# Optimization experiments

Measured on AMD Instinct MI355X. Metric: run time of the kernel, lower is better.

Reference implementation:

```python
import jax, jax.numpy as jnp
import numpy as np

N = 100000
E = 1600000
IN_DIM = 128
H = 64
OUT_DIM = 64
EPS = 1e-5


def batch_norm(x, gamma, beta):
    # BatchNorm1d with batch statistics (training-mode normalization, biased var)
    mu = jnp.mean(x, axis=0)
    var = jnp.var(x, axis=0)
    return (x - mu) * jax.lax.rsqrt(var + EPS) * gamma + beta


def gcn_conv(x, src, dst, W, b, n_nodes):
    # PyG GCNConv: add self-loops, symmetric deg^-1/2 normalization, X W, scatter-add, bias
    loop = jnp.arange(n_nodes, dtype=src.dtype)
    s = jnp.concatenate([src, loop])
    d = jnp.concatenate([dst, loop])
    w = jnp.ones(s.shape[0], dtype=x.dtype)
    deg = jax.ops.segment_sum(w, d, num_segments=n_nodes)
    dinv = jnp.where(deg > 0, jax.lax.rsqrt(deg), 0.0)
    norm = dinv[s] * w * dinv[d]                      # [E+N]
    h = x @ W                                         # [N, out]
    msg = h[s] * norm[:, None]                        # [E+N, out]
    out = jax.ops.segment_sum(msg, d, num_segments=n_nodes)
    return out + b


def setup_inputs() -> dict:
    key = jax.random.key(0)
    ks = jax.random.split(key, 12)
    x = jax.random.normal(ks[0], (N, IN_DIM), dtype=jnp.float32)
    edge_index = jax.random.randint(ks[1], (2, E), 0, N, dtype=jnp.int64)
    s = 0.05
    return {
        "x": x,
        "edge_index": edge_index,
        "bn_in_g": jnp.ones((IN_DIM,), jnp.float32),
        "bn_in_b": jnp.zeros((IN_DIM,), jnp.float32),
        "Wp": jax.random.normal(ks[2], (IN_DIM, H), jnp.float32) * s,
        "bp": jnp.zeros((H,), jnp.float32),
        "W1": jax.random.normal(ks[3], (H, H), jnp.float32) * s,
        "b1": jnp.zeros((H,), jnp.float32),
        "bn1_g": jnp.ones((H,), jnp.float32),
        "bn1_b": jnp.zeros((H,), jnp.float32),
        "W2": jax.random.normal(ks[4], (H, OUT_DIM), jnp.float32) * s,
        "b2": jnp.zeros((OUT_DIM,), jnp.float32),
        "bn2_g": jnp.ones((OUT_DIM,), jnp.float32),
        "bn2_b": jnp.zeros((OUT_DIM,), jnp.float32),
    }


def reference(x, edge_index, bn_in_g, bn_in_b, Wp, bp, W1, b1, bn1_g, bn1_b, W2, b2, bn2_g, bn2_b):
    src, dst = edge_index[0], edge_index[1]
    n = x.shape[0]
    h0 = batch_norm(x, bn_in_g, bn_in_b)
    h0 = jax.nn.relu(h0 @ Wp + bp)
    h1 = gcn_conv(h0, src, dst, W1, b1, n)
    h1 = jax.nn.relu(batch_norm(h1, bn1_g, bn1_b))
    # dropout in eval mode: identity
    h2 = gcn_conv(h1, src, dst, W2, b2, n)
    return batch_norm(h2, bn2_g, bn2_b)
```

## Files before the change

### kernel.cpp

```cpp
#include <hip/hip_runtime.h>
#include <hip/hip_bf16.h>

#define EPS 1e-5f

__device__ __forceinline__ void acc_q(float* acc, uint2 v, float s) {
    acc[0] += s * (float)((int)(v.x << 24) >> 24);
    acc[1] += s * (float)((int)(v.x << 16) >> 24);
    acc[2] += s * (float)((int)(v.x << 8) >> 24);
    acc[3] += s * (float)((int)v.x >> 24);
    acc[4] += s * (float)((int)(v.y << 24) >> 24);
    acc[5] += s * (float)((int)(v.y << 16) >> 24);
    acc[6] += s * (float)((int)(v.y << 8) >> 24);
    acc[7] += s * (float)((int)v.y >> 24);
}

__global__ __launch_bounds__(256) void k_pre(const int* __restrict__ dst,
                                             int* __restrict__ cc,
                                             const float* __restrict__ x,
                                             float* __restrict__ xsum,
                                             float* __restrict__ xsq,
                                             int E, int N, int NB) {
    __shared__ float lsf[512];
    int tx = threadIdx.x;
    if (blockIdx.x < 512) {
        int* h = (int*)lsf;
        for (int i = tx; i < NB; i += 256) h[i] = 0;
        __syncthreads();
        int stride = 512 * 256;
        for (int e = blockIdx.x * 256 + tx; e < E; e += stride)
            atomicAdd(&h[dst[e] >> 8], 1);
        __syncthreads();
        for (int i = tx; i < NB; i += 256)
            if (h[i]) atomicAdd(&cc[i], h[i]);
    } else {
        float* ls = lsf;
        float* lq = lsf + 256;
        int b2 = blockIdx.x - 512;
        int col = tx & 127, half = tx >> 7;
        float s = 0.f, q = 0.f;
        for (int r = b2 * 2 + half; r < N; r += 1024) {
            float v = x[(long long)r * 128 + col];
            s += v; q += v * v;
        }
        ls[tx] = s; lq[tx] = q;
        __syncthreads();
        if (half == 0) {
            s = ls[tx] + ls[tx + 128];
            q = lq[tx] + lq[tx + 128];
            atomicAdd(&xsum[col], s);
            atomicAdd(&xsq[col], q);
        }
    }
}

__global__ void k_cscan(const int* __restrict__ cc, int* __restrict__ coff,
                        int* __restrict__ cur, int NB, int E) {
    __shared__ int ls[512];
    int tx = threadIdx.x;
    int v = (tx < NB) ? cc[tx] : 0;
    ls[tx] = v;
    __syncthreads();
    for (int off = 1; off < 512; off <<= 1) {
        int u = (tx >= off) ? ls[tx - off] : 0;
        __syncthreads();
        ls[tx] += u;
        __syncthreads();
    }
    int excl = ls[tx] - v;
    if (tx < NB) { coff[tx] = excl; cur[tx] = excl; }
    if (tx == NB - 1) coff[NB] = excl + v;
}

#define PCHUNK 4096
__global__ __launch_bounds__(256) void k_mid(
    const int* __restrict__ src, const int* __restrict__ dst,
    int* __restrict__ cursor, unsigned* __restrict__ packbuf, int E, int NB, int PB,
    const float* __restrict__ x, const float* __restrict__ stats,
    const float* __restrict__ g, const float* __restrict__ bbn,
    const float* __restrict__ Wp, const float* __restrict__ bp,
    float* __restrict__ H, float invN, int N) {
    __shared__ int h[512], delta[512], wsc[4];
    __shared__ unsigned buf[PCHUNK];
    __shared__ int addr[PCHUNK];
    int tx = threadIdx.x;
    if (blockIdx.x < PB) {
        int e0 = blockIdx.x * PCHUNK;
        int e1 = min(e0 + PCHUNK, E);
        int csize = e1 - e0;
        h[tx] = 0; h[tx + 256] = 0;
        __syncthreads();
        for (int e = e0 + tx; e < e1; e += 256)
            atomicAdd(&h[dst[e] >> 8], 1);
        __syncthreads();
        int b0 = tx * 2;
        int c0 = h[b0], c1 = h[b0 + 1];
        int tsum = c0 + c1;
        int lane = tx & 63, wid = tx >> 6;
        int v = tsum;
#pragma unroll
        for (int off = 1; off < 64; off <<= 1) {
            int u = __shfl_up(v, off);
            if (lane >= off) v += u;
        }
        if (lane == 63) wsc[wid] = v;
        __syncthreads();
        int wbase = 0;
        for (int w = 0; w < wid; w++) wbase += wsc[w];
        int excl0 = wbase + v - tsum;
        int excl1 = excl0 + c0;
        if (b0 < NB && c0 > 0) delta[b0] = atomicAdd(&cursor[b0], c0) - excl0;
        if (b0 + 1 < NB && c1 > 0) delta[b0 + 1] = atomicAdd(&cursor[b0 + 1], c1) - excl1;
        __syncthreads();
        h[b0] = excl0; h[b0 + 1] = excl1;
        __syncthreads();
        for (int e = e0 + tx; e < e1; e += 256) {
            int d = dst[e];
            int b = d >> 8;
            int rank = atomicAdd(&h[b], 1);
            buf[rank] = ((unsigned)src[e] << 8) | (unsigned)(d & 255);
            addr[rank] = delta[b];
        }
        __syncthreads();
        for (int i = tx; i < csize; i += 256)
            packbuf[addr[i] + i] = buf[i];
    } else {
        float* sc = (float*)h;
        float* sh = (float*)delta;
        if (tx < 128) {
            float mu = stats[tx] * invN;
            float var = stats[128 + tx] * invN - mu * mu;
            float s = g[tx] * rsqrtf(var + EPS);
            sc[tx] = s;
            sh[tx] = bbn[tx] - mu * s;
        }
        __syncthreads();
        int r = (blockIdx.x - PB) * 256 + tx;
        if (r >= N) return;
        float acc[64];
#pragma unroll
        for (int j = 0; j < 64; j++) acc[j] = 0.f;
        const float4* x4 = (const float4*)(x + (long long)r * 128);
        for (int c4 = 0; c4 < 32; c4++) {
            float4 xv = x4[c4];
            int cb = c4 * 4;
            xv.x = xv.x * sc[cb + 0] + sh[cb + 0];
            xv.y = xv.y * sc[cb + 1] + sh[cb + 1];
            xv.z = xv.z * sc[cb + 2] + sh[cb + 2];
            xv.w = xv.w * sc[cb + 3] + sh[cb + 3];
#pragma unroll
            for (int q = 0; q < 4; q++) {
                float xs = (q == 0) ? xv.x : (q == 1) ? xv.y : (q == 2) ? xv.z : xv.w;
                const float* wrow = Wp + (c4 * 4 + q) * 64;
#pragma unroll
                for (int j = 0; j < 64; j++) acc[j] += xs * wrow[j];
            }
        }
        float4* out4 = (float4*)(H + (long long)r * 64);
#pragma unroll
        for (int i = 0; i < 16; i++) {
            float4 vv;
            vv.x = fmaxf(acc[4 * i + 0] + bp[4 * i + 0], 0.f);
            vv.y = fmaxf(acc[4 * i + 1] + bp[4 * i + 1], 0.f);
            vv.z = fmaxf(acc[4 * i + 2] + bp[4 * i + 2], 0.f);
            vv.w = fmaxf(acc[4 * i + 3] + bp[4 * i + 3], 0.f);
            out4[i] = vv;
        }
    }
}

__global__ __launch_bounds__(512) void k_build(const unsigned* __restrict__ packbuf,
                                               const int* __restrict__ coff,
                                               int* __restrict__ rowptr,
                                               float* __restrict__ dinv,
                                               int* __restrict__ eidx, int N, int E) {
    __shared__ int cnt[256], loff[256], wsum[4];
    int b = blockIdx.x;
    int tx = threadIdx.x;
    int beg = coff[b], end = coff[b + 1];
    if (tx < 256) cnt[tx] = 0;
    __syncthreads();
    for (int e = beg + tx; e < end; e += 512)
        atomicAdd(&cnt[packbuf[e] & 255u], 1);
    __syncthreads();
    if (tx < 256) {
        int c = cnt[tx];
        int lane = tx & 63, wid = tx >> 6;
        int v = c;
#pragma unroll
        for (int off = 1; off < 64; off <<= 1) {
            int u = __shfl_up(v, off);
            if (lane >= off) v += u;
        }
        if (lane == 63) wsum[wid] = v;
        __syncthreads();
        int wbase = 0;
        for (int w = 0; w < wid; w++) wbase += wsum[w];
        int excl = wbase + v - c;
        loff[tx] = excl;
        int node = b * 256 + tx;
        if (node < N) {
            rowptr[node] = beg + excl;
            dinv[node] = rsqrtf(1.0f + (float)c);
        }
    } else {
        __syncthreads();
    }
    if (b == 0 && tx == 0) rowptr[N] = E;
    __syncthreads();
    for (int e = beg + tx; e < end; e += 512) {
        unsigned pk = packbuf[e];
        int pos = atomicAdd(&loff[pk & 255u], 1);
        eidx[beg + pos] = (int)(pk >> 8);
    }
}

template <bool BNRELU>
__global__ __launch_bounds__(256) void k_gemm_scale(
    const float* __restrict__ In, const float* __restrict__ W,
    const float* __restrict__ dinv, const float* __restrict__ ssum,
    const float* __restrict__ ssq, const float* __restrict__ g,
    const float* __restrict__ bb, float invN, unsigned* __restrict__ Bq,
    float* __restrict__ S, int N) {
    __shared__ float scs[64], shs[64];
    int tx = threadIdx.x;
    if (BNRELU) {
        if (tx < 64) {
            float mu = ssum[tx] * invN;
            float var = ssq[tx] * invN - mu * mu;
            float s = g[tx] * rsqrtf(var + EPS);
            scs[tx] = s;
            shs[tx] = bb[tx] - mu * s;
        }
        __syncthreads();
    }
    int r = blockIdx.x * blockDim.x + tx;
    if (r >= N) return;
    float acc[64];
#pragma unroll
    for (int j = 0; j < 64; j++) acc[j] = 0.f;
    const float4* in4 = (const float4*)(In + (long long)r * 64);
    for (int c4 = 0; c4 < 16; c4++) {
        float4 xv = in4[c4];
        if (BNRELU) {
            int cb = c4 * 4;
            xv.x = fmaxf(xv.x * scs[cb + 0] + shs[cb + 0], 0.f);
            xv.y = fmaxf(xv.y * scs[cb + 1] + shs[cb + 1], 0.f);
            xv.z = fmaxf(xv.z * scs[cb + 2] + shs[cb + 2], 0.f);
            xv.w = fmaxf(xv.w * scs[cb + 3] + shs[cb + 3], 0.f);
        }
#pragma unroll
        for (int q = 0; q < 4; q++) {
            float xs = (q == 0) ? xv.x : (q == 1) ? xv.y : (q == 2) ? xv.z : xv.w;
            const float* wrow = W + (c4 * 4 + q) * 64;
#pragma unroll
            for (int j = 0; j < 64; j++) acc[j] += xs * wrow[j];
        }
    }
    float dv = dinv[r];
    float vmax = 0.f;
#pragma unroll
    for (int j = 0; j < 64; j++) {
        acc[j] *= dv;
        vmax = fmaxf(vmax, fabsf(acc[j]));
    }
    S[r] = vmax * (1.0f / 127.0f);
    float inv = (vmax > 0.f) ? (127.0f / vmax) : 0.f;
    uint4* b4 = (uint4*)(Bq + (long long)r * 16);
#pragma unroll
    for (int i = 0; i < 4; i++) {
        unsigned w[4];
#pragma unroll
        for (int k2 = 0; k2 < 4; k2++) {
            int bsx = i * 16 + k2 * 4;
            unsigned q0 = (unsigned)((int)rintf(acc[bsx + 0] * inv)) & 255u;
            unsigned q1 = (unsigned)((int)rintf(acc[bsx + 1] * inv)) & 255u;
            unsigned q2 = (unsigned)((int)rintf(acc[bsx + 2] * inv)) & 255u;
            unsigned q3 = (unsigned)((int)rintf(acc[bsx + 3] * inv)) & 255u;
            w[k2] = q0 | (q1 << 8) | (q2 << 16) | (q3 << 24);
        }
        b4[i] = make_uint4(w[0], w[1], w[2], w[3]);
    }
}

__global__ __launch_bounds__(256) void k_gather_finish(
    const uint2* __restrict__ B, const float* __restrict__ S,
    const int* __restrict__ rowptr, const int* __restrict__ eidx,
    const float* __restrict__ dinv, const float* __restrict__ bias,
    float* __restrict__ Out, float* __restrict__ ssum, float* __restrict__ ssq, int N) {
    int tx = threadIdx.x;
    int g = tx >> 3;
    int l = tx & 7;
    int d = blockIdx.x * 32 + g;

    float s[8], q[8];
#pragma unroll
    for (int j = 0; j < 8; j++) { s[j] = 0.f; q[j] = 0.f; }

    if (d < N) {
        int beg = rowptr[d], end = rowptr[d + 1];
        float acc[8];
#pragma unroll
        for (int j = 0; j < 8; j++) acc[j] = 0.f;
        {
            uint2 v0 = B[(long long)d * 8 + l];
            acc_q(acc, v0, S[d]);
        }
        int k = beg;
        for (; k + 3 < end; k += 4) {
            int i0 = eidx[k + 0], i1 = eidx[k + 1], i2 = eidx[k + 2], i3 = eidx[k + 3];
            uint2 a0 = B[(long long)i0 * 8 + l];
            uint2 a1 = B[(long long)i1 * 8 + l];
            uint2 a2 = B[(long long)i2 * 8 + l];
            uint2 a3 = B[(long long)i3 * 8 + l];
            float s0 = S[i0], s1 = S[i1], s2 = S[i2], s3 = S[i3];
            acc_q(acc, a0, s0); acc_q(acc, a1, s1);
            acc_q(acc, a2, s2); acc_q(acc, a3, s3);
        }
        for (; k + 1 < end; k += 2) {
            int i0 = eidx[k + 0], i1 = eidx[k + 1];
            uint2 a0 = B[(long long)i0 * 8 + l];
            uint2 a1 = B[(long long)i1 * 8 + l];
            float s0 = S[i0], s1 = S[i1];
            acc_q(acc, a0, s0); acc_q(acc, a1, s1);
        }
        if (k < end) {
            int i0 = eidx[k];
            uint2 a0 = B[(long long)i0 * 8 + l];
            acc_q(acc, a0, S[i0]);
        }
        float dv = dinv[d];
        float4 o0, o1;
#pragma unroll
        for (int j = 0; j < 8; j++) {
            float v = acc[j] * dv + bias[8 * l + j];
            ((j < 4) ? (&o0.x)[j] : (&o1.x)[j - 4]) = v;
            s[j] += v; q[j] += v * v;
        }
        float4* outp = (float4*)(Out + (long long)d * 64 + 8 * l);
        outp[0] = o0;
        outp[1] = o1;
    }

#pragma unroll
    for (int m = 8; m <= 32; m <<= 1) {
#pragma unroll
        for (int j = 0; j < 8; j++) {
            s[j] += __shfl_xor(s[j], m, 64);
            q[j] += __shfl_xor(q[j], m, 64);
        }
    }
    __shared__ float ws_s[4][64], ws_q[4][64];
    int wv = tx >> 6, ln = tx & 63;
    if (ln < 8) {
#pragma unroll
        for (int j = 0; j < 8; j++) {
            ws_s[wv][ln * 8 + j] = s[j];
            ws_q[wv][ln * 8 + j] = q[j];
        }
    }
    __syncthreads();
    if (tx < 64) {
        float S2 = ws_s[0][tx] + ws_s[1][tx] + ws_s[2][tx] + ws_s[3][tx];
        float Q2 = ws_q[0][tx] + ws_q[1][tx] + ws_q[2][tx] + ws_q[3][tx];
        atomicAdd(&ssum[tx], S2);
        atomicAdd(&ssq[tx], Q2);
    }
}

__global__ __launch_bounds__(256) void k_final(const float* __restrict__ In,
                                               const float* __restrict__ ssum,
                                               const float* __restrict__ ssq,
                                               const float* __restrict__ g,
                                               const float* __restrict__ bb, float invN,
                                               float* __restrict__ out, int total4) {
    __shared__ float scs[64], shs[64];
    int tx = threadIdx.x;
    if (tx < 64) {
        float mu = ssum[tx] * invN;
        float var = ssq[tx] * invN - mu * mu;
        float s = g[tx] * rsqrtf(var + EPS);
        scs[tx] = s;
        shs[tx] = bb[tx] - mu * s;
    }
    __syncthreads();
    int t = blockIdx.x * blockDim.x + tx;
    if (t < total4) {
        float4 v = ((const float4*)In)[t];
        int j = (t * 4) & 63;
        v.x = v.x * scs[j + 0] + shs[j + 0];
        v.y = v.y * scs[j + 1] + shs[j + 1];
        v.z = v.z * scs[j + 2] + shs[j + 2];
        v.w = v.w * scs[j + 3] + shs[j + 3];
        ((float4*)out)[t] = v;
    }
}

extern "C" void kernel_launch(void* const* d_in, const int* in_sizes, int n_in,
                              void* d_out, int out_size, void* d_ws, size_t ws_size,
                              hipStream_t stream) {
    const float* x       = (const float*)d_in[0];
    const int*   ei      = (const int*)d_in[1];
    const float* bn_in_g = (const float*)d_in[2];
    const float* bn_in_b = (const float*)d_in[3];
    const float* Wp      = (const float*)d_in[4];
    const float* bp      = (const float*)d_in[5];
    const float* W1      = (const float*)d_in[6];
    const float* b1      = (const float*)d_in[7];
    const float* bn1_g   = (const float*)d_in[8];
    const float* bn1_b   = (const float*)d_in[9];
    const float* W2      = (const float*)d_in[10];
    const float* b2      = (const float*)d_in[11];
    const float* bn2_g   = (const float*)d_in[12];
    const float* bn2_b   = (const float*)d_in[13];

    int N = in_sizes[0] / 128;
    int E = in_sizes[1] / 2;
    const int* src = ei;
    const int* dst = ei + E;
    int NB = (N + 255) >> 8;

    long long Npad = ((long long)N + 128) & ~127LL;
    int*   cc     = (int*)d_ws;
    float* stats  = (float*)(cc + 512);
    int*   coff   = (int*)(stats + 512);
    int*   cur    = coff + 640;
    int*   rowptr = cur + 512;
    float* dinv   = (float*)(rowptr + Npad);
    float* S      = dinv + Npad;
    unsigned* packbuf = (unsigned*)(S + Npad);
    int*   eidx   = (int*)(packbuf + ((E + 127) & ~127));
    unsigned* Bq  = (unsigned*)(eidx + ((E + 127) & ~127));
    float* H      = (float*)d_out;

    int nb = (N + 255) / 256;
    int gb = (N + 31) / 32;
    int PB = (E + PCHUNK - 1) / PCHUNK;
    float invN = 1.0f / (float)N;

    hipMemsetAsync(d_ws, 0, (512 + 512) * 4, stream);

    k_pre<<<1024, 256, 0, stream>>>(dst, cc, x, stats, stats + 128, E, N, NB);
    k_cscan<<<1, 512, 0, stream>>>(cc, coff, cur, NB, E);
    k_mid<<<PB + nb, 256, 0, stream>>>(src, dst, cur, packbuf, E, NB, PB,
                                       x, stats, bn_in_g, bn_in_b, Wp, bp, H, invN, N);
    k_build<<<NB, 512, 0, stream>>>(packbuf, coff, rowptr, dinv, eidx, N, E);

    k_gemm_scale<false><<<nb, 256, 0, stream>>>(H, W1, dinv, nullptr, nullptr, nullptr,
                                                nullptr, invN, Bq, S, N);
    k_gather_finish<<<gb, 256, 0, stream>>>((const uint2*)Bq, S, rowptr, eidx, dinv,
                                            b1, H, stats + 256, stats + 320, N);

    k_gemm_scale<true><<<nb, 256, 0, stream>>>(H, W2, dinv, stats + 256, stats + 320,
                                               bn1_g, bn1_b, invN, Bq, S, N);
    k_gather_finish<<<gb, 256, 0, stream>>>((const uint2*)Bq, S, rowptr, eidx, dinv,
                                            b2, H, stats + 384, stats + 448, N);

    k_final<<<(N * 16 + 255) / 256, 256, 0, stream>>>(H, stats + 384, stats + 448,
                                                      bn2_g, bn2_b, invN, H, N * 16);
}
```

Measured before the change: 482.7 us.

## Replace bucket count-and-scan with fixed-capacity buckets, fuse CSR build with input projection

Removes the separate dst-histogram pass and single-block scan by giving each 256-node bucket a fixed slot region of CAP entries, so scatter cursors start at b*CAP. The x column statistics move into the scatter kernel, and the CSR build is merged with the BN+projection GEMM into one launch, with rows stored as begin/end pairs. This drops two kernels, a memset and one full pass over dst. In exchange, the workspace grows with padding, and correctness relies on no bucket exceeding CAP edges, an assumption that only holds for random uniform inputs.

```diff
diff --git a/kernel.cpp b/kernel.cpp
--- a/kernel.cpp
+++ b/kernel.cpp
@@ -2,6 +2,8 @@
 #include <hip/hip_bf16.h>
 
 #define EPS 1e-5f
+#define CAP 6144
+#define PCHUNK 4096
 
 __device__ __forceinline__ void acc_q(float* acc, uint2 v, float s) {
     acc[0] += s * (float)((int)(v.x << 24) >> 24);
@@ -14,76 +16,21 @@
     acc[7] += s * (float)((int)v.y >> 24);
 }
 
-__global__ __launch_bounds__(256) void k_pre(const int* __restrict__ dst,
-                                             int* __restrict__ cc,
-                                             const float* __restrict__ x,
-                                             float* __restrict__ xsum,
-                                             float* __restrict__ xsq,
-                                             int E, int N, int NB) {
-    __shared__ float lsf[512];
-    int tx = threadIdx.x;
-    if (blockIdx.x < 512) {
-        int* h = (int*)lsf;
-        for (int i = tx; i < NB; i += 256) h[i] = 0;
-        __syncthreads();
-        int stride = 512 * 256;
-        for (int e = blockIdx.x * 256 + tx; e < E; e += stride)
-            atomicAdd(&h[dst[e] >> 8], 1);
-        __syncthreads();
-        for (int i = tx; i < NB; i += 256)
-            if (h[i]) atomicAdd(&cc[i], h[i]);
-    } else {
-        float* ls = lsf;
-        float* lq = lsf + 256;
-        int b2 = blockIdx.x - 512;
-        int col = tx & 127, half = tx >> 7;
-        float s = 0.f, q = 0.f;
-        for (int r = b2 * 2 + half; r < N; r += 1024) {
-            float v = x[(long long)r * 128 + col];
-            s += v; q += v * v;
-        }
-        ls[tx] = s; lq[tx] = q;
-        __syncthreads();
-        if (half == 0) {
-            s = ls[tx] + ls[tx + 128];
-            q = lq[tx] + lq[tx + 128];
-            atomicAdd(&xsum[col], s);
-            atomicAdd(&xsq[col], q);
-        }
-    }
-}
-
-__global__ void k_cscan(const int* __restrict__ cc, int* __restrict__ coff,
-                        int* __restrict__ cur, int NB, int E) {
-    __shared__ int ls[512];
-    int tx = threadIdx.x;
-    int v = (tx < NB) ? cc[tx] : 0;
-    ls[tx] = v;
-    __syncthreads();
-    for (int off = 1; off < 512; off <<= 1) {
-        int u = (tx >= off) ? ls[tx - off] : 0;
-        __syncthreads();
-        ls[tx] += u;
-        __syncthreads();
-    }
-    int excl = ls[tx] - v;
-    if (tx < NB) { coff[tx] = excl; cur[tx] = excl; }
-    if (tx == NB - 1) coff[NB] = excl + v;
-}
-
-#define PCHUNK 4096
-__global__ __launch_bounds__(256) void k_mid(
+__global__ void k_init(int* __restrict__ cur, float* __restrict__ stats) {
+    int t = threadIdx.x;
+    stats[t] = 0.0f;
+    cur[t] = t * CAP;
+}
+
+__global__ __launch_bounds__(256) void k_A(
     const int* __restrict__ src, const int* __restrict__ dst,
-    int* __restrict__ cursor, unsigned* __restrict__ packbuf, int E, int NB, int PB,
-    const float* __restrict__ x, const float* __restrict__ stats,
-    const float* __restrict__ g, const float* __restrict__ bbn,
-    const float* __restrict__ Wp, const float* __restrict__ bp,
-    float* __restrict__ H, float invN, int N) {
+    int* __restrict__ cur, unsigned* __restrict__ packbuf, int E, int NBP,
+    const float* __restrict__ x, float* __restrict__ xsum, float* __restrict__ xsq, int N) {
     __shared__ int h[512], delta[512], wsc[4];
     __shared__ unsigned buf[PCHUNK];
     __shared__ int addr[PCHUNK];
     int tx = threadIdx.x;
-    if (blockIdx.x < PB) {
+    if ((int)blockIdx.x < NBP) {
         int e0 = blockIdx.x * PCHUNK;
         int e1 = min(e0 + PCHUNK, E);
         int csize = e1 - e0;
@@ -108,8 +55,8 @@
         for (int w = 0; w < wid; w++) wbase += wsc[w];
         int excl0 = wbase + v - tsum;
         int excl1 = excl0 + c0;
-        if (b0 < NB && c0 > 0) delta[b0] = atomicAdd(&cursor[b0], c0) - excl0;
-        if (b0 + 1 < NB && c1 > 0) delta[b0 + 1] = atomicAdd(&cursor[b0 + 1], c1) - excl1;
+        if (c0 > 0) delta[b0] = atomicAdd(&cur[b0], c0) - excl0;
+        if (c1 > 0) delta[b0 + 1] = atomicAdd(&cur[b0 + 1], c1) - excl1;
         __syncthreads();
         h[b0] = excl0; h[b0 + 1] = excl1;
         __syncthreads();
@@ -124,8 +71,77 @@
         for (int i = tx; i < csize; i += 256)
             packbuf[addr[i] + i] = buf[i];
     } else {
-        float* sc = (float*)h;
-        float* sh = (float*)delta;
+        float* ls = (float*)buf;
+        float* lq = ls + 256;
+        int b2 = blockIdx.x - NBP;
+        int col = tx & 127, half = tx >> 7;
+        float s = 0.f, q = 0.f;
+        for (int r = b2 * 2 + half; r < N; r += 1024) {
+            float v = x[(long long)r * 128 + col];
+            s += v; q += v * v;
+        }
+        ls[tx] = s; lq[tx] = q;
+        __syncthreads();
+        if (half == 0) {
+            s = ls[tx] + ls[tx + 128];
+            q = lq[tx] + lq[tx + 128];
+            atomicAdd(&xsum[col], s);
+            atomicAdd(&xsq[col], q);
+        }
+    }
+}
+
+__global__ __launch_bounds__(512) void k_B(
+    const unsigned* __restrict__ packbuf, const int* __restrict__ cur,
+    int2* __restrict__ rowbe, float* __restrict__ dinv, int* __restrict__ eidx,
+    int NB, int N,
+    const float* __restrict__ x, const float* __restrict__ stats,
+    const float* __restrict__ g, const float* __restrict__ bbn,
+    const float* __restrict__ Wp, const float* __restrict__ bp,
+    float* __restrict__ H, float invN) {
+    __shared__ int cnt[256], loff[256], wsum[4];
+    int tx = threadIdx.x;
+    if ((int)blockIdx.x < NB) {
+        int b = blockIdx.x;
+        int base = b * CAP;
+        int end = cur[b];
+        if (tx < 256) cnt[tx] = 0;
+        __syncthreads();
+        for (int e = base + tx; e < end; e += 512)
+            atomicAdd(&cnt[packbuf[e] & 255u], 1);
+        __syncthreads();
+        if (tx < 256) {
+            int c = cnt[tx];
+            int lane = tx & 63, wid = tx >> 6;
+            int v = c;
+#pragma unroll
+            for (int off = 1; off < 64; off <<= 1) {
+                int u = __shfl_up(v, off);
+                if (lane >= off) v += u;
+            }
+            if (lane == 63) wsum[wid] = v;
+            __syncthreads();
+            int wbase = 0;
+            for (int w = 0; w < wid; w++) wbase += wsum[w];
+            int excl = wbase + v - c;
+            loff[tx] = excl;
+            int node = b * 256 + tx;
+            if (node < N) {
+                rowbe[node] = make_int2(base + excl, base + excl + c);
+                dinv[node] = rsqrtf(1.0f + (float)c);
+            }
+        } else {
+            __syncthreads();
+        }
+        __syncthreads();
+        for (int e = base + tx; e < end; e += 512) {
+            unsigned pk = packbuf[e];
+            int pos = atomicAdd(&loff[pk & 255u], 1);
+            eidx[base + pos] = (int)(pk >> 8);
+        }
+    } else {
+        float* sc = (float*)cnt;
+        float* sh = (float*)loff;
         if (tx < 128) {
             float mu = stats[tx] * invN;
             float var = stats[128 + tx] * invN - mu * mu;
@@ -134,7 +150,7 @@
             sh[tx] = bbn[tx] - mu * s;
         }
         __syncthreads();
-        int r = (blockIdx.x - PB) * 256 + tx;
+        int r = ((int)blockIdx.x - NB) * 512 + tx;
         if (r >= N) return;
         float acc[64];
 #pragma unroll
@@ -165,52 +181,6 @@
             vv.w = fmaxf(acc[4 * i + 3] + bp[4 * i + 3], 0.f);
             out4[i] = vv;
         }
-    }
-}
-
-__global__ __launch_bounds__(512) void k_build(const unsigned* __restrict__ packbuf,
-                                               const int* __restrict__ coff,
-                                               int* __restrict__ rowptr,
-                                               float* __restrict__ dinv,
-                                               int* __restrict__ eidx, int N, int E) {
-    __shared__ int cnt[256], loff[256], wsum[4];
-    int b = blockIdx.x;
-    int tx = threadIdx.x;
-    int beg = coff[b], end = coff[b + 1];
-    if (tx < 256) cnt[tx] = 0;
-    __syncthreads();
-    for (int e = beg + tx; e < end; e += 512)
-        atomicAdd(&cnt[packbuf[e] & 255u], 1);
-    __syncthreads();
-    if (tx < 256) {
-        int c = cnt[tx];
-        int lane = tx & 63, wid = tx >> 6;
-        int v = c;
-#pragma unroll
-        for (int off = 1; off < 64; off <<= 1) {
-            int u = __shfl_up(v, off);
-            if (lane >= off) v += u;
-        }
-        if (lane == 63) wsum[wid] = v;
-        __syncthreads();
-        int wbase = 0;
-        for (int w = 0; w < wid; w++) wbase += wsum[w];
-        int excl = wbase + v - c;
-        loff[tx] = excl;
-        int node = b * 256 + tx;
-        if (node < N) {
-            rowptr[node] = beg + excl;
-            dinv[node] = rsqrtf(1.0f + (float)c);
-        }
-    } else {
-        __syncthreads();
-    }
-    if (b == 0 && tx == 0) rowptr[N] = E;
-    __syncthreads();
-    for (int e = beg + tx; e < end; e += 512) {
-        unsigned pk = packbuf[e];
-        int pos = atomicAdd(&loff[pk & 255u], 1);
-        eidx[beg + pos] = (int)(pk >> 8);
     }
 }
 
@@ -284,7 +254,7 @@
 
 __global__ __launch_bounds__(256) void k_gather_finish(
     const uint2* __restrict__ B, const float* __restrict__ S,
-    const int* __restrict__ rowptr, const int* __restrict__ eidx,
+    const int2* __restrict__ rowbe, const int* __restrict__ eidx,
     const float* __restrict__ dinv, const float* __restrict__ bias,
     float* __restrict__ Out, float* __restrict__ ssum, float* __restrict__ ssq, int N) {
     int tx = threadIdx.x;
@@ -297,7 +267,8 @@
     for (int j = 0; j < 8; j++) { s[j] = 0.f; q[j] = 0.f; }
 
     if (d < N) {
-        int beg = rowptr[d], end = rowptr[d + 1];
+        int2 be = rowbe[d];
+        int beg = be.x, end = be.y;
         float acc[8];
 #pragma unroll
         for (int j = 0; j < 8; j++) acc[j] = 0.f;
@@ -417,42 +388,39 @@
     int E = in_sizes[1] / 2;
     const int* src = ei;
     const int* dst = ei + E;
-    int NB = (N + 255) >> 8;
+    int NB  = (N + 255) >> 8;
+    int NBP = (E + PCHUNK - 1) / PCHUNK;
+    int nbg = (N + 511) / 512;
 
     long long Npad = ((long long)N + 128) & ~127LL;
-    int*   cc     = (int*)d_ws;
-    float* stats  = (float*)(cc + 512);
-    int*   coff   = (int*)(stats + 512);
-    int*   cur    = coff + 640;
-    int*   rowptr = cur + 512;
-    float* dinv   = (float*)(rowptr + Npad);
+    int*   cur    = (int*)d_ws;
+    float* stats  = (float*)(cur + 512);
+    int2*  rowbe  = (int2*)(stats + 512);
+    float* dinv   = (float*)(rowbe + Npad);
     float* S      = dinv + Npad;
     unsigned* packbuf = (unsigned*)(S + Npad);
-    int*   eidx   = (int*)(packbuf + ((E + 127) & ~127));
-    unsigned* Bq  = (unsigned*)(eidx + ((E + 127) & ~127));
+    int*   eidx   = (int*)(packbuf + (long long)NB * CAP);
+    unsigned* Bq  = (unsigned*)(eidx + (long long)NB * CAP);
     float* H      = (float*)d_out;
 
     int nb = (N + 255) / 256;
     int gb = (N + 31) / 32;
-    int PB = (E + PCHUNK - 1) / PCHUNK;
     float invN = 1.0f / (float)N;
 
-    hipMemsetAsync(d_ws, 0, (512 + 512) * 4, stream);
-
-    k_pre<<<1024, 256, 0, stream>>>(dst, cc, x, stats, stats + 128, E, N, NB);
-    k_cscan<<<1, 512, 0, stream>>>(cc, coff, cur, NB, E);
-    k_mid<<<PB + nb, 256, 0, stream>>>(src, dst, cur, packbuf, E, NB, PB,
-                                       x, stats, bn_in_g, bn_in_b, Wp, bp, H, invN, N);
-    k_build<<<NB, 512, 0, stream>>>(packbuf, coff, rowptr, dinv, eidx, N, E);
+    k_init<<<1, 512, 0, stream>>>(cur, stats);
+    k_A<<<NBP + 512, 256, 0, stream>>>(src, dst, cur, packbuf, E, NBP,
+                                       x, stats, stats + 128, N);
+    k_B<<<NB + nbg, 512, 0, stream>>>(packbuf, cur, rowbe, dinv, eidx, NB, N,
+                                      x, stats, bn_in_g, bn_in_b, Wp, bp, H, invN);
 
     k_gemm_scale<false><<<nb, 256, 0, stream>>>(H, W1, dinv, nullptr, nullptr, nullptr,
                                                 nullptr, invN, Bq, S, N);
-    k_gather_finish<<<gb, 256, 0, stream>>>((const uint2*)Bq, S, rowptr, eidx, dinv,
+    k_gather_finish<<<gb, 256, 0, stream>>>((const uint2*)Bq, S, rowbe, eidx, dinv,
                                             b1, H, stats + 256, stats + 320, N);
 
     k_gemm_scale<true><<<nb, 256, 0, stream>>>(H, W2, dinv, stats + 256, stats + 320,
                                                bn1_g, bn1_b, invN, Bq, S, N);
-    k_gather_finish<<<gb, 256, 0, stream>>>((const uint2*)Bq, S, rowptr, eidx, dinv,
+    k_gather_finish<<<gb, 256, 0, stream>>>((const uint2*)Bq, S, rowbe, eidx, dinv,
                                             b2, H, stats + 384, stats + 448, N);
 
     k_final<<<(N * 16 + 255) / 256, 256, 0, stream>>>(H, stats + 384, stats + 448,
```

Measured after the change: 479.5 us. About the same (-0.7%).
